# Optimization experiments

Measured on AMD Instinct MI355X. Metric: run time of the kernel, lower is better.

The kernel has to match this reference:

```python
import jax, jax.numpy as jnp
import numpy as np

BN_EPS = 1e-5


def setup_inputs() -> dict:
    key = jax.random.key(0)
    ks = jax.random.split(key, 16)
    B, C, H, W = 8, 256, 56, 56
    Ci = C // 2  # inter_channels = 128
    s = lambda fan_in: 1.0 / np.sqrt(fan_in)
    return {
        "x": jax.random.normal(ks[0], (B, C, H, W), jnp.float32),
        # 1x1 convs stored as [out, in] matrices
        "g_w": jax.random.normal(ks[1], (Ci, C), jnp.float32) * s(C),
        "g_b": jax.random.normal(ks[2], (Ci,), jnp.float32) * s(C),
        "theta_w": jax.random.normal(ks[3], (Ci, C), jnp.float32) * s(C),
        "theta_b": jax.random.normal(ks[4], (Ci,), jnp.float32) * s(C),
        "phi_w": jax.random.normal(ks[5], (Ci, C), jnp.float32) * s(C),
        "phi_b": jax.random.normal(ks[6], (Ci,), jnp.float32) * s(C),
        # W_f: Conv2d(2*Ci -> 1, k=1)
        "wf_w": jax.random.normal(ks[7], (1, 2 * Ci), jnp.float32) * s(2 * Ci),
        "wf_b": jax.random.normal(ks[8], (1,), jnp.float32) * s(2 * Ci),
        # W_z conv (Ci -> C); source zero-inits; random here for a non-trivial baseline
        "wz_w": jax.random.normal(ks[9], (C, Ci), jnp.float32) * s(Ci),
        "wz_b": jax.random.normal(ks[10], (C,), jnp.float32) * s(Ci),
        # BatchNorm2d (eval mode) params/stats; source zero-inits gamma/beta, randomized here
        "bn_gamma": jax.random.normal(ks[11], (C,), jnp.float32) * 0.1 + 1.0,
        "bn_beta": jax.random.normal(ks[12], (C,), jnp.float32) * 0.1,
        "bn_mean": jax.random.normal(ks[13], (C,), jnp.float32) * 0.1,
        "bn_var": jax.random.uniform(ks[14], (C,), jnp.float32, 0.5, 1.5),
    }


def reference(x, g_w, g_b, theta_w, theta_b, phi_w, phi_b,
              wf_w, wf_b, wz_w, wz_b, bn_gamma, bn_beta, bn_mean, bn_var):
    B, C, H, W = x.shape
    N = H * W
    Ci = g_w.shape[0]
    xf = x.reshape(B, C, N)  # [B, C, N]

    # 1x1 convs over flattened spatial dim
    g_x = jnp.einsum('oc,bcn->bno', g_w, xf) + g_b            # [B, N, Ci]
    theta = jnp.einsum('oc,bcn->bon', theta_w, xf) + theta_b[:, None]  # [B, Ci, N]
    phi = jnp.einsum('oc,bcn->bon', phi_w, xf) + phi_b[:, None]        # [B, Ci, N]

    # W_f over the (repeat+concat) tensor decomposes exactly:
    # f[b,i,j] = relu( w_t . theta[b,:,i] + w_p . phi[b,:,j] + b_f )
    w_t, w_p = wf_w[0, :Ci], wf_w[0, Ci:]
    a = jnp.einsum('c,bcn->bn', w_t, theta)   # [B, N]
    bsc = jnp.einsum('c,bcn->bn', w_p, phi)   # [B, N]
    f = jax.nn.relu(a[:, :, None] + bsc[:, None, :] + wf_b[0])  # [B, N, N]

    y = jnp.matmul(f / N, g_x)                # [B, N, Ci]
    y = y.transpose(0, 2, 1)                  # [B, Ci, N]

    W_y = jnp.einsum('oc,bcn->bon', wz_w, y) + wz_b[:, None]   # [B, C, N]
    inv = bn_gamma / jnp.sqrt(bn_var + BN_EPS)
    W_y = (W_y - bn_mean[:, None]) * inv[:, None] + bn_beta[:, None]

    z = W_y + xf
    return z.reshape(B, C, H, W)
```

## Files before the change

### kernel.cpp

```cpp
#include <hip/hip_runtime.h>
#include <cfloat>
#include <math.h>

#define BATCH 8
#define CH 256
#define CI 128
#define NPIX 3136
#define NCHUNK 98
#define NB 4096
#define BN_EPS 1e-5f

typedef __attribute__((ext_vector_type(8))) short bf16x8;
typedef __attribute__((ext_vector_type(4))) float f32x4;

__device__ __forceinline__ float bf2f(unsigned short u) {
    union { unsigned int i; float f; } x; x.i = ((unsigned int)u) << 16; return x.f;
}
__device__ __forceinline__ unsigned short f2bf(float f) {
    union { float f; unsigned int i; } x; x.f = f;
    unsigned int u = x.i;
    return (unsigned short)((u + 0x7FFFu + ((u >> 16) & 1u)) >> 16);
}

__global__ __launch_bounds__(256) void k_fold(
    const float* __restrict__ wf_w,
    const float* __restrict__ theta_w, const float* __restrict__ theta_b,
    const float* __restrict__ phi_w,   const float* __restrict__ phi_b,
    const float* __restrict__ g_w,     const float* __restrict__ wz_w,
    float* __restrict__ ta_w, float* __restrict__ pb_w, float* __restrict__ biases,
    unsigned short* __restrict__ Bfrag_g, unsigned short* __restrict__ Bfrag_w)
{
    const int bk = blockIdx.x, tid = threadIdx.x;
    if (bk == 0) {
        float ta = 0.f, pb = 0.f;
        for (int c = 0; c < CI; ++c) {
            ta += wf_w[c]      * theta_w[c * CH + tid];
            pb += wf_w[CI + c] * phi_w[c * CH + tid];
        }
        ta_w[tid] = ta;
        pb_w[tid] = pb;
        if (tid == 0) {
            float tb = 0.f, pbb = 0.f;
            for (int c = 0; c < CI; ++c) {
                tb  += wf_w[c]      * theta_b[c];
                pbb += wf_w[CI + c] * phi_b[c];
            }
            biases[0] = tb;
            biases[1] = pbb;
        }
    } else if (bk <= 8) {
        const int base_pair = (bk - 1) * 8;
        for (int e = tid; e < 4096; e += 256) {
            int pp = e >> 9, lane = (e >> 3) & 63, j = e & 7;
            int pair = base_pair + pp;
            int ks = pair >> 3, nt = pair & 7;
            int k = ks * 32 + (lane >> 4) * 8 + j;
            int n = nt * 16 + (lane & 15);
            Bfrag_g[(size_t)pair * 512 + lane * 8 + j] = f2bf(g_w[n * CH + k]);
        }
    } else {
        const int base_pair = (bk - 9) * 8;
        for (int e = tid; e < 4096; e += 256) {
            int pp = e >> 9, lane = (e >> 3) & 63, j = e & 7;
            int pair = base_pair + pp;
            int ks = pair >> 4, nt = pair & 15;
            int k = ks * 32 + (lane >> 4) * 8 + j;
            int n = nt * 16 + (lane & 15);
            Bfrag_w[(size_t)pair * 512 + lane * 8 + j] = f2bf(wz_w[n * CI + k]);
        }
    }
}

__global__ __launch_bounds__(256) void k_gemm(
    const float* __restrict__ x,
    const unsigned short* __restrict__ Bfrag_g,
    const float* __restrict__ g_b,
    const float* __restrict__ ta_w, const float* __restrict__ pb_w,
    const float* __restrict__ biases,
    unsigned short* __restrict__ gxg,
    float* __restrict__ a_out, float* __restrict__ bsc_out)
{
    __shared__ float xs[CH][36];
    __shared__ unsigned short xsb[64 * 264];
    __shared__ float ra[8][32], rp[8][32];
    unsigned short* gout = (unsigned short*)&xs[0][0];

    const int b  = blockIdx.y;
    const int n0 = blockIdx.x * 64;
    const int tid = threadIdx.x;
    const int p = tid & 31;
    const int g = tid >> 5;

    for (int half = 0; half < 2; ++half) {
        for (int t = tid; t < CH * 8; t += 256) {
            int c = t >> 3, n4 = t & 7;
            const float4* src = (const float4*)(x + ((size_t)b * CH + c) * NPIX + n0 + half * 32);
            *((float4*)&xs[c][n4 * 4]) = src[n4];
        }
        __syncthreads();

        {
            const int cbase = g * 32;
            float aa = 0.f, pp = 0.f;
            unsigned int* dst = (unsigned int*)&xsb[(half * 32 + p) * 264 + cbase];
#pragma unroll
            for (int q = 0; q < 16; ++q) {
                int c0 = cbase + 2 * q;
                float lo = xs[c0][p];
                float hi = xs[c0 + 1][p];
                aa += ta_w[c0] * lo + ta_w[c0 + 1] * hi;
                pp += pb_w[c0] * lo + pb_w[c0 + 1] * hi;
                dst[q] = (unsigned int)f2bf(lo) | ((unsigned int)f2bf(hi) << 16);
            }
            ra[g][p] = aa; rp[g][p] = pp;
        }
        __syncthreads();

        if (tid < 32) {
            float sa = 0.f, sp = 0.f;
#pragma unroll
            for (int gg = 0; gg < 8; ++gg) { sa += ra[gg][tid]; sp += rp[gg][tid]; }
            a_out[b * NPIX + n0 + half * 32 + tid]   = sa + biases[0];
            bsc_out[b * NPIX + n0 + half * 32 + tid] = sp + biases[1];
        }
    }

    const int w = tid >> 6, l = tid & 63, lm = l & 15, lq = l >> 4;
    f32x4 acc[4][2];
#pragma unroll
    for (int mi = 0; mi < 4; ++mi)
#pragma unroll
        for (int ni = 0; ni < 2; ++ni) acc[mi][ni] = (f32x4){0.f, 0.f, 0.f, 0.f};

#pragma unroll
    for (int ks = 0; ks < 8; ++ks) {
        bf16x8 b0 = *(const bf16x8*)(Bfrag_g + ((size_t)(ks * 8 + w * 2) * 64 + l) * 8);
        bf16x8 b1 = *(const bf16x8*)(Bfrag_g + ((size_t)(ks * 8 + w * 2 + 1) * 64 + l) * 8);
#pragma unroll
        for (int mi = 0; mi < 4; ++mi) {
            bf16x8 a0 = *(const bf16x8*)&xsb[(mi * 16 + lm) * 264 + ks * 32 + lq * 8];
            acc[mi][0] = __builtin_amdgcn_mfma_f32_16x16x32_bf16(a0, b0, acc[mi][0], 0, 0, 0);
            acc[mi][1] = __builtin_amdgcn_mfma_f32_16x16x32_bf16(a0, b1, acc[mi][1], 0, 0, 0);
        }
    }

#pragma unroll
    for (int mi = 0; mi < 4; ++mi)
#pragma unroll
        for (int ni = 0; ni < 2; ++ni) {
            int o = w * 32 + ni * 16 + lm;
            float gb = g_b[o];
#pragma unroll
            for (int r = 0; r < 4; ++r) {
                int m = mi * 16 + lq * 4 + r;
                gout[m * 136 + o] = f2bf(acc[mi][ni][r] + gb);
            }
        }
    __syncthreads();

    {
        const int n = tid >> 2, ch = tid & 3;
        const uint4* s = (const uint4*)&gout[n * 136 + ch * 32];
        uint4* d = (uint4*)(gxg + ((size_t)(b * NPIX + n0 + n)) * CI + ch * 32);
        d[0] = s[0]; d[1] = s[1]; d[2] = s[2]; d[3] = s[3];
    }
}

__global__ __launch_bounds__(1024) void k_bucketsort(
    const float* __restrict__ bsc,
    float* __restrict__ s_sorted, int* __restrict__ idx_sorted,
    int* __restrict__ bstart, float* __restrict__ params)
{
    __shared__ int hist[NB];
    __shared__ int cnt[NB];
    __shared__ float wmin[16], wmax[16];
    __shared__ int wtot[16], woff[16];
    __shared__ float sh_min, sh_scale;

    const int b = blockIdx.x, tid = threadIdx.x;
    const int lane = tid & 63, wid = tid >> 6;

#pragma unroll
    for (int k = 0; k < 4; ++k) { hist[tid + k * 1024] = 0; cnt[tid + k * 1024] = 0; }

    float v[4];
    float lmin = FLT_MAX, lmax = -FLT_MAX;
#pragma unroll
    for (int k = 0; k < 4; ++k) {
        int i = tid + k * 1024;
        if (i < NPIX) {
            float t = bsc[b * NPIX + i];
            v[k] = t;
            lmin = fminf(lmin, t);
            lmax = fmaxf(lmax, t);
        }
    }
#pragma unroll
    for (int m = 32; m >= 1; m >>= 1) {
        lmin = fminf(lmin, __shfl_xor(lmin, m));
        lmax = fmaxf(lmax, __shfl_xor(lmax, m));
    }
    if (lane == 0) { wmin[wid] = lmin; wmax[wid] = lmax; }
    __syncthreads();

    if (tid < 16) {
        float a = wmin[tid], c = wmax[tid];
#pragma unroll
        for (int m = 8; m >= 1; m >>= 1) {
            a = fminf(a, __shfl_xor(a, m));
            c = fmaxf(c, __shfl_xor(c, m));
        }
        if (tid == 0) {
            float range = c - a;
            float scale = (range > 0.f) ? (float)NB / range : 0.f;
            sh_min = a; sh_scale = scale;
            params[b * 2] = a; params[b * 2 + 1] = scale;
        }
    }
    __syncthreads();

    const float bmin = sh_min, scale = sh_scale;
    int q[4];
#pragma unroll
    for (int k = 0; k < 4; ++k) {
        int i = tid + k * 1024;
        if (i < NPIX) {
            int qq = (int)((v[k] - bmin) * scale);
            qq = (qq < 0) ? 0 : ((qq > NB - 1) ? NB - 1 : qq);
            q[k] = qq;
            atomicAdd(&hist[qq], 1);
        }
    }
    __syncthreads();

    const int base4 = tid * 4;
    int h0 = hist[base4], h1 = hist[base4 + 1], h2 = hist[base4 + 2], h3 = hist[base4 + 3];
    int s = h0 + h1 + h2 + h3;
    int incl = s;
#pragma unroll
    for (int off = 1; off < 64; off <<= 1) {
        int t = __shfl_up(incl, off);
        if (lane >= off) incl += t;
    }
    if (lane == 63) wtot[wid] = incl;
    __syncthreads();
    if (tid < 16) {
        int t = wtot[tid];
        int wi = t;
#pragma unroll
        for (int off = 1; off < 16; off <<= 1) {
            int u = __shfl_up(wi, off);
            if (tid >= off) wi += u;
        }
        woff[tid] = wi - t;
    }
    __syncthreads();
    int excl = woff[wid] + (incl - s);
    hist[base4]     = excl;
    hist[base4 + 1] = excl + h0;
    hist[base4 + 2] = excl + h0 + h1;
    hist[base4 + 3] = excl + h0 + h1 + h2;
    __syncthreads();

#pragma unroll
    for (int k = 0; k < 4; ++k) {
        int i = tid + k * 1024;
        bstart[b * (NB + 1) + i] = hist[i];
    }
    if (tid == 0) bstart[b * (NB + 1) + NB] = NPIX;

#pragma unroll
    for (int k = 0; k < 4; ++k) {
        int i = tid + k * 1024;
        if (i < NPIX) {
            int pos = hist[q[k]] + atomicAdd(&cnt[q[k]], 1);
            s_sorted[b * NPIX + pos]   = v[k];
            idx_sorted[b * NPIX + pos] = i;
        }
    }
}

__global__ __launch_bounds__(64) void k_csum(
    const unsigned short* __restrict__ gxg,
    const float* __restrict__ s_sorted, const int* __restrict__ idx_sorted,
    float* __restrict__ CS1, float* __restrict__ CS2)
{
    const int b = blockIdx.y, c = blockIdx.x, t = threadIdx.x;
    const int base = b * NPIX + c * 32;

    int   my_i = idx_sorted[base + (t & 31)];
    float my_v = s_sorted[base + (t & 31)];

    float a1x = 0.f, a1y = 0.f, a2x = 0.f, a2y = 0.f;
#pragma unroll 8
    for (int rr = 0; rr < 32; ++rr) {
        int   row = __shfl(my_i, rr);
        float sv  = __shfl(my_v, rr);
        unsigned int u = *(const unsigned int*)(gxg + ((size_t)(b * NPIX + row)) * CI + 2 * t);
        float v0 = bf2f((unsigned short)(u & 0xffffu));
        float v1 = bf2f((unsigned short)(u >> 16));
        a1x += v0;      a1y += v1;
        a2x += sv * v0; a2y += sv * v1;
    }
    float2* p1 = (float2*)&CS1[(b * 100 + c) * CI];
    float2* p2 = (float2*)&CS2[(b * 100 + c) * CI];
    p1[t] = make_float2(a1x, a1y);
    p2[t] = make_float2(a2x, a2y);
}

__global__ __launch_bounds__(1024) void k_suffix(
    float* __restrict__ CS1, float* __restrict__ CS2)
{
    __shared__ float buf[NCHUNK * CI];
    __shared__ float tot[8][CI];
    const int b = blockIdx.x, tid = threadIdx.x;
    float* __restrict__ CS = blockIdx.y ? CS2 : CS1;

    for (int i = tid; i < NCHUNK * CI; i += 1024) buf[i] = CS[b * 100 * CI + i];
    __syncthreads();

    const int seg = tid >> 7, o = tid & 127;
    const int c0 = seg * 13;
    const int c1 = (seg == 7) ? NCHUNK : c0 + 13;
    {
        float acc = 0.f;
        for (int c = c1 - 1; c >= c0; --c) {
            acc += buf[c * CI + o];
            buf[c * CI + o] = acc;
        }
        tot[seg][o] = acc;
    }
    __syncthreads();
    {
        float off = 0.f;
#pragma unroll
        for (int s2 = 7; s2 >= 1; --s2) if (s2 > seg) off += tot[s2][o];
        if (off != 0.f || seg < 7) {
            for (int c = c0; c < c1; ++c) buf[c * CI + o] += off;
        }
    }
    __syncthreads();
    for (int i = tid; i < NCHUNK * CI; i += 1024) CS[b * 100 * CI + i] = buf[i];
    if (tid < CI) {
        CS[(b * 100 + 98) * CI + tid] = 0.f;
        CS[(b * 100 + 99) * CI + tid] = 0.f;
    }
}

__global__ __launch_bounds__(256) void k_final(
    const float* __restrict__ x,
    const float* __restrict__ a_arr, const float* __restrict__ wf_b,
    const float* __restrict__ CS1, const float* __restrict__ CS2,
    const int* __restrict__ bstart, const float* __restrict__ params,
    const unsigned short* __restrict__ Bfrag_w,
    const float* __restrict__ wz_b,
    const float* __restrict__ bn_g, const float* __restrict__ bn_b,
    const float* __restrict__ bn_m, const float* __restrict__ bn_v,
    float* __restrict__ out)
{
    __shared__ unsigned short ys[64 * 136];
    __shared__ int   rs[64];
    __shared__ float ts[64];

    const int b = blockIdx.y;
    const int n0 = blockIdx.x * 64;
    const int tid = threadIdx.x;

    if (tid < 64) {
        float t = a_arr[b * NPIX + n0 + tid] + wf_b[0];
        float bmin = params[b * 2], scale = params[b * 2 + 1];
        float fq = (-t - bmin) * scale;
        int kb = (int)(fq + 0.5f);
        kb = (kb < 0) ? 0 : ((kb > NB) ? NB : kb);
        int r = bstart[b * (NB + 1) + kb];
        int cstar = (r + 16) >> 5;
        cstar = (cstar > 98) ? 98 : cstar;
        rs[tid] = cstar;
        ts[tid] = t;
    }
    __syncthreads();

    const int o = tid & 127;
    const int h = tid >> 7;
    const float invN = 1.0f / (float)NPIX;

#pragma unroll 4
    for (int i = 0; i < 32; ++i) {
        int n = h * 32 + i;
        int cb = (b * 100 + rs[n]) * CI + o;
        float S1 = CS1[cb], S2 = CS2[cb];
        ys[n * 136 + o] = f2bf((ts[n] * S1 + S2) * invN);
    }
    __syncthreads();

    const int w = tid >> 6, l = tid & 63, lm = l & 15, lq = l >> 4;

    float invv[4], biasv[4];
#pragma unroll
    for (int ni = 0; ni < 4; ++ni) {
        int cc = w * 64 + ni * 16 + lm;
        float iv = bn_g[cc] * rsqrtf(bn_v[cc] + BN_EPS);
        invv[ni] = iv;
        biasv[ni] = (wz_b[cc] - bn_m[cc]) * iv + bn_b[cc];
    }

    f32x4 acc[4][4];
#pragma unroll
    for (int mi = 0; mi < 4; ++mi)
#pragma unroll
        for (int ni = 0; ni < 4; ++ni) acc[mi][ni] = (f32x4){0.f, 0.f, 0.f, 0.f};

#pragma unroll
    for (int ks = 0; ks < 4; ++ks) {
        bf16x8 af[4];
#pragma unroll
        for (int mi = 0; mi < 4; ++mi)
            af[mi] = *(const bf16x8*)&ys[(mi * 16 + lm) * 136 + ks * 32 + lq * 8];
#pragma unroll
        for (int ni = 0; ni < 4; ++ni) {
            bf16x8 bb = *(const bf16x8*)(Bfrag_w + ((size_t)(ks * 16 + w * 4 + ni) * 64 + l) * 8);
#pragma unroll
            for (int mi = 0; mi < 4; ++mi)
                acc[mi][ni] = __builtin_amdgcn_mfma_f32_16x16x32_bf16(af[mi], bb, acc[mi][ni], 0, 0, 0);
        }
    }

#pragma unroll
    for (int mi = 0; mi < 4; ++mi)
#pragma unroll
        for (int ni = 0; ni < 4; ++ni) {
            int cc = w * 64 + ni * 16 + lm;
            int m  = mi * 16 + lq * 4;
            size_t base = ((size_t)b * CH + cc) * NPIX + n0 + m;
            const float4 xv = *(const float4*)(x + base);
            float4 ov;
            ov.x = acc[mi][ni][0] * invv[ni] + biasv[ni] + xv.x;
            ov.y = acc[mi][ni][1] * invv[ni] + biasv[ni] + xv.y;
            ov.z = acc[mi][ni][2] * invv[ni] + biasv[ni] + xv.z;
            ov.w = acc[mi][ni][3] * invv[ni] + biasv[ni] + xv.w;
            *(float4*)(out + base) = ov;
        }
}

extern "C" void kernel_launch(void* const* d_in, const int* in_sizes, int n_in,
                              void* d_out, int out_size, void* d_ws, size_t ws_size,
                              hipStream_t stream)
{
    const float* x       = (const float*)d_in[0];
    const float* g_w     = (const float*)d_in[1];
    const float* g_b     = (const float*)d_in[2];
    const float* theta_w = (const float*)d_in[3];
    const float* theta_b = (const float*)d_in[4];
    const float* phi_w   = (const float*)d_in[5];
    const float* phi_b   = (const float*)d_in[6];
    const float* wf_w    = (const float*)d_in[7];
    const float* wf_b    = (const float*)d_in[8];
    const float* wz_w    = (const float*)d_in[9];
    const float* wz_b    = (const float*)d_in[10];
    const float* bn_g    = (const float*)d_in[11];
    const float* bn_b    = (const float*)d_in[12];
    const float* bn_m    = (const float*)d_in[13];
    const float* bn_v    = (const float*)d_in[14];

    float* ws = (float*)d_ws;
    float* ta_w   = ws;
    float* pb_w   = ws + 256;
    float* biases = ws + 512;
    float* params = ws + 516;
    float* a_arr  = ws + 532;
    float* bsc      = a_arr + BATCH * NPIX;
    float* s_sorted = bsc + BATCH * NPIX;
    int*   idx_sorted = (int*)(s_sorted + BATCH * NPIX);
    int*   bstart   = idx_sorted + BATCH * NPIX;
    float* CS1    = (float*)(bstart + BATCH * (NB + 1));
    float* CS2    = CS1 + BATCH * 100 * CI;
    unsigned short* Bfrag_g = (unsigned short*)(CS2 + BATCH * 100 * CI);
    unsigned short* Bfrag_w = Bfrag_g + 32768;
    unsigned short* gxg = Bfrag_w + 32768;

    k_fold<<<17, 256, 0, stream>>>(wf_w, theta_w, theta_b, phi_w, phi_b,
                                   g_w, wz_w, ta_w, pb_w, biases,
                                   Bfrag_g, Bfrag_w);

    k_gemm<<<dim3(49, BATCH), 256, 0, stream>>>(
        x, Bfrag_g, g_b, ta_w, pb_w, biases, gxg, a_arr, bsc);

    k_bucketsort<<<BATCH, 1024, 0, stream>>>(bsc, s_sorted, idx_sorted,
                                             bstart, params);

    k_csum<<<dim3(NCHUNK, BATCH), 64, 0, stream>>>(
        gxg, s_sorted, idx_sorted, CS1, CS2);

    k_suffix<<<dim3(BATCH, 2), 1024, 0, stream>>>(CS1, CS2);

    k_final<<<dim3(49, BATCH), 256, 0, stream>>>(
        x, a_arr, wf_b, CS1, CS2, bstart, params, Bfrag_w,
        wz_b, bn_g, bn_b, bn_m, bn_v, (float*)d_out);
}
```

Before: 153.7 us.

## Load x directly into MFMA A-fragments in registers, skipping LDS staging

The g-projection GEMM kernel no longer stages x tiles through shared memory. Each wave now reads its own 16 pixels straight from global memory into bf16 A-fragments in registers, and computes the theta/phi dot products with wave shuffles. The work split changes so each wave owns 16 rows across all 128 output channels, instead of 64 rows by 32 channels. This removes the LDS traffic and two barriers per half-tile, and shrinks shared memory. The cost is more global B-fragment loads per wave, higher register use, and strided per-channel global reads of x.

```diff
diff --git a/kernel.cpp b/kernel.cpp
--- a/kernel.cpp
+++ b/kernel.cpp
@@ -80,82 +80,65 @@
     unsigned short* __restrict__ gxg,
     float* __restrict__ a_out, float* __restrict__ bsc_out)
 {
-    __shared__ float xs[CH][36];
-    __shared__ unsigned short xsb[64 * 264];
-    __shared__ float ra[8][32], rp[8][32];
-    unsigned short* gout = (unsigned short*)&xs[0][0];
+    __shared__ unsigned short gout[64 * 136];
 
     const int b  = blockIdx.y;
     const int n0 = blockIdx.x * 64;
     const int tid = threadIdx.x;
-    const int p = tid & 31;
-    const int g = tid >> 5;
-
-    for (int half = 0; half < 2; ++half) {
-        for (int t = tid; t < CH * 8; t += 256) {
-            int c = t >> 3, n4 = t & 7;
-            const float4* src = (const float4*)(x + ((size_t)b * CH + c) * NPIX + n0 + half * 32);
-            *((float4*)&xs[c][n4 * 4]) = src[n4];
-        }
-        __syncthreads();
-
-        {
-            const int cbase = g * 32;
-            float aa = 0.f, pp = 0.f;
-            unsigned int* dst = (unsigned int*)&xsb[(half * 32 + p) * 264 + cbase];
-#pragma unroll
-            for (int q = 0; q < 16; ++q) {
-                int c0 = cbase + 2 * q;
-                float lo = xs[c0][p];
-                float hi = xs[c0 + 1][p];
-                aa += ta_w[c0] * lo + ta_w[c0 + 1] * hi;
-                pp += pb_w[c0] * lo + pb_w[c0 + 1] * hi;
-                dst[q] = (unsigned int)f2bf(lo) | ((unsigned int)f2bf(hi) << 16);
-            }
-            ra[g][p] = aa; rp[g][p] = pp;
-        }
-        __syncthreads();
-
-        if (tid < 32) {
-            float sa = 0.f, sp = 0.f;
-#pragma unroll
-            for (int gg = 0; gg < 8; ++gg) { sa += ra[gg][tid]; sp += rp[gg][tid]; }
-            a_out[b * NPIX + n0 + half * 32 + tid]   = sa + biases[0];
-            bsc_out[b * NPIX + n0 + half * 32 + tid] = sp + biases[1];
-        }
-    }
-
     const int w = tid >> 6, l = tid & 63, lm = l & 15, lq = l >> 4;
-    f32x4 acc[4][2];
-#pragma unroll
-    for (int mi = 0; mi < 4; ++mi)
-#pragma unroll
-        for (int ni = 0; ni < 2; ++ni) acc[mi][ni] = (f32x4){0.f, 0.f, 0.f, 0.f};
-
+    const int px = n0 + w * 16 + lm;
+
+    const float* xb = x + (size_t)b * CH * NPIX + px;
+
+    bf16x8 af[8];
+    float aa = 0.f, pp = 0.f;
 #pragma unroll
     for (int ks = 0; ks < 8; ++ks) {
-        bf16x8 b0 = *(const bf16x8*)(Bfrag_g + ((size_t)(ks * 8 + w * 2) * 64 + l) * 8);
-        bf16x8 b1 = *(const bf16x8*)(Bfrag_g + ((size_t)(ks * 8 + w * 2 + 1) * 64 + l) * 8);
-#pragma unroll
-        for (int mi = 0; mi < 4; ++mi) {
-            bf16x8 a0 = *(const bf16x8*)&xsb[(mi * 16 + lm) * 264 + ks * 32 + lq * 8];
-            acc[mi][0] = __builtin_amdgcn_mfma_f32_16x16x32_bf16(a0, b0, acc[mi][0], 0, 0, 0);
-            acc[mi][1] = __builtin_amdgcn_mfma_f32_16x16x32_bf16(a0, b1, acc[mi][1], 0, 0, 0);
-        }
-    }
-
-#pragma unroll
-    for (int mi = 0; mi < 4; ++mi)
-#pragma unroll
-        for (int ni = 0; ni < 2; ++ni) {
-            int o = w * 32 + ni * 16 + lm;
-            float gb = g_b[o];
-#pragma unroll
-            for (int r = 0; r < 4; ++r) {
-                int m = mi * 16 + lq * 4 + r;
-                gout[m * 136 + o] = f2bf(acc[mi][ni][r] + gb);
-            }
-        }
+        float v[8];
+#pragma unroll
+        for (int j = 0; j < 8; ++j) {
+            int c = ks * 32 + lq * 8 + j;
+            float t = xb[(size_t)c * NPIX];
+            v[j] = t;
+            aa += ta_w[c] * t;
+            pp += pb_w[c] * t;
+        }
+        union { bf16x8 v8; unsigned short u[8]; } pk;
+#pragma unroll
+        for (int j = 0; j < 8; ++j) pk.u[j] = f2bf(v[j]);
+        af[ks] = pk.v8;
+    }
+
+    aa += __shfl_xor(aa, 16); aa += __shfl_xor(aa, 32);
+    pp += __shfl_xor(pp, 16); pp += __shfl_xor(pp, 32);
+    if (l < 16) {
+        a_out[b * NPIX + px]   = aa + biases[0];
+        bsc_out[b * NPIX + px] = pp + biases[1];
+    }
+
+    f32x4 acc[8];
+#pragma unroll
+    for (int nt = 0; nt < 8; ++nt) acc[nt] = (f32x4){0.f, 0.f, 0.f, 0.f};
+
+#pragma unroll
+    for (int ks = 0; ks < 8; ++ks) {
+#pragma unroll
+        for (int nt = 0; nt < 8; ++nt) {
+            bf16x8 bb = *(const bf16x8*)(Bfrag_g + ((size_t)(ks * 8 + nt) * 64 + l) * 8);
+            acc[nt] = __builtin_amdgcn_mfma_f32_16x16x32_bf16(af[ks], bb, acc[nt], 0, 0, 0);
+        }
+    }
+
+#pragma unroll
+    for (int nt = 0; nt < 8; ++nt) {
+        int o = nt * 16 + lm;
+        float gb = g_b[o];
+#pragma unroll
+        for (int r = 0; r < 4; ++r) {
+            int m = w * 16 + lq * 4 + r;
+            gout[m * 136 + o] = f2bf(acc[nt][r] + gb);
+        }
+    }
     __syncthreads();
 
     {
```

New measurement: 153.7 us. No clear change (-0.1%).
